# Optimization experiments

Hardware: AMD Instinct MI355X
Metric: run time of the kernel (lower is better)

## Reference

```python
import jax, jax.numpy as jnp
import numpy as np

L, C, B = 256, 20, 1024


def _pos_mask(L):
    # pairwise mask: l2 - l1 >= 1, shape (L, L); broadcast over channels
    ls = jnp.arange(L)
    return (ls[None, :] - ls[:, None]) >= 1


def setup_inputs() -> dict:
    key = jax.random.key(0)
    k0, k1, k2 = jax.random.split(key, 3)
    x_lc = jax.random.uniform(k0, (B, L, C), dtype=jnp.float32)
    theta_0 = jnp.zeros((1,), dtype=jnp.float32)
    theta_lc = jax.random.normal(k1, (1, L, C), dtype=jnp.float32) / np.sqrt(L)
    pm = _pos_mask(L)
    theta_lclc = (jax.random.normal(k2, (1, L, C, L, C), dtype=jnp.float32)
                  / np.sqrt(L * L)) * pm[None, :, None, :, None]
    mask = pm
    return {"x_lc": x_lc, "theta_0": theta_0, "theta_lc": theta_lc,
            "theta_lclc": theta_lclc, "mask": mask}


def reference(x_lc, theta_0, theta_lc, theta_lclc, mask):
    Bn = x_lc.shape[0]
    # additive term: sum_{l,c} theta_lc * x
    phi = theta_0 + jnp.einsum('blc,zlc->b', x_lc, theta_lc)[:, None]
    # pairwise term as a masked bilinear form: x^T (mask * theta) x
    # (avoids materializing the (B,L,C,L,C) broadcast of the original)
    theta_m = theta_lclc[0] * mask[:, None, :, None].astype(theta_lclc.dtype)
    LC = L * C
    xf = x_lc.reshape(Bn, LC)                      # (B, LC)
    tf_ = theta_m.reshape(LC, LC)                  # (LC, LC)
    pair = jnp.einsum('bi,ij,bj->b', xf, tf_, xf)  # two GEMMs under the hood
    phi = phi + pair[:, None]
    return phi
```

## Files before the change

kernel.cpp:

```cpp
#include <hip/hip_runtime.h>
#include <stdint.h>

#define LDIM 256
#define CDIM 20
#define LC   5120
#define NB   1024
#define BM   128
#define BN   256
#define ITOT64 1640

typedef __attribute__((ext_vector_type(8))) short short8;
typedef __attribute__((ext_vector_type(4))) float float4v;
typedef __attribute__((ext_vector_type(4))) unsigned int uint4v;
typedef unsigned short ushort_t;

#define XB_BYTES (10485760ull)
#define WS_NEED  (XB_BYTES)

__device__ inline uint32_t pack_bf16x2(float a, float b) {
    uint32_t ua = __float_as_uint(a);
    uint32_t ub = __float_as_uint(b);
    ua += 0x7fffu + ((ua >> 16) & 1u);
    ub += 0x7fffu + ((ub >> 16) & 1u);
    return (ua >> 16) | (ub & 0xffff0000u);
}

__device__ inline float bf16_to_f32(ushort_t u) {
    return __uint_as_float(((uint32_t)u) << 16);
}

__device__ inline void load_lds16(const void* g, void* l) {
    __builtin_amdgcn_global_load_lds(
        (const __attribute__((address_space(1))) uint32_t*)g,
        (__attribute__((address_space(3))) uint32_t*)l, 16, 0, 0);
}

__global__ __launch_bounds__(256) void xconv_kernel(
    const float* __restrict__ X, const float* __restrict__ th0,
    const float* __restrict__ thlc, ushort_t* __restrict__ Xb,
    float* __restrict__ out)
{
    const int b = blockIdx.x;
    const int t = threadIdx.x;
    __shared__ float red[4];

    const float*  src = X  + (size_t)b * LC;
    ushort_t*     dst = Xb + (size_t)b * LC;
    float s = 0.f;
    for (int c = t * 4; c < LC; c += 1024) {
        float4 f = *(const float4*)(src + c);
        float4 w = *(const float4*)(thlc + c);
        s += f.x * w.x + f.y * w.y + f.z * w.z + f.w * w.w;
        uint2 u;
        u.x = pack_bf16x2(f.x, f.y);
        u.y = pack_bf16x2(f.z, f.w);
        *(uint2*)(dst + c) = u;
    }
    s += __shfl_xor(s, 1);  s += __shfl_xor(s, 2);  s += __shfl_xor(s, 4);
    s += __shfl_xor(s, 8);  s += __shfl_xor(s, 16); s += __shfl_xor(s, 32);
    if ((t & 63) == 0) red[t >> 6] = s;
    __syncthreads();
    if (t == 0) out[b] = th0[0] + red[0] + red[1] + red[2] + red[3];
}

__global__ __launch_bounds__(256, 2) void pair_fused(
    const float* __restrict__ T, const ushort_t* __restrict__ Xb,
    float* __restrict__ out)
{
    const int n    = blockIdx.x;
    const int kblk = ((n >> 3) << 1) | (n & 1);
    const int bn0  = ((n >> 1) & 3) * BN;

    const int gbeg = (ITOT64 * kblk) >> 7;
    const int gend = (ITOT64 * (kblk + 1)) >> 7;

    int it = 0, pre = 0;
    while (pre + (80 - 2 * it) <= gbeg) { pre += 80 - 2 * it; ++it; }
    int li = gbeg - pre;

    __shared__ __align__(16) ushort_t A_s[1024 * 8];
    __shared__ __align__(16) ushort_t B_s[2][2048 * 8];

    const int t    = threadIdx.x;
    const int lane = t & 63;
    const int wid  = t >> 6;
    const int wm   = (wid >> 1) * 64;
    const int wn   = (wid & 1) * 128;
    const int l16  = lane & 15;
    const int qk   = lane >> 4;

    const int r32 = t >> 3;
    const int ga  = t & 7;
    uint32_t offTa[4];
    int      wAdr[4];
    #pragma unroll
    for (int j = 0; j < 4; ++j) {
        const int row = r32 + j * 32;
        offTa[j] = (uint32_t)row * LC + (ga << 3);
        wAdr[j]  = ((row << 3) + (ga ^ (row & 7))) << 4;
    }

    uint32_t offB[8];
    #pragma unroll
    for (int j = 0; j < 8; ++j) {
        const int c = (wid << 9) + (j << 6) + lane;
        const int row = c >> 3;
        const int g2 = (c & 7) ^ (row & 7);
        offB[j] = (uint32_t)(bn0 + row) * LC + (g2 << 3);
    }

    int adrA[2][4], adrB[2][8];
    #pragma unroll
    for (int step = 0; step < 2; ++step) {
        const int kf = step * 4 + qk;
        #pragma unroll
        for (int mt = 0; mt < 4; ++mt) {
            const int r = wm + mt * 16 + l16;
            adrA[step][mt] = ((r << 3) + (kf ^ (r & 7))) << 4;
        }
        #pragma unroll
        for (int nt = 0; nt < 8; ++nt) {
            const int r = wn + nt * 16 + l16;
            adrB[step][nt] = ((r << 3) + (kf ^ (r & 7))) << 4;
        }
    }

    int i0 = it << 7;
    int k0 = i0 + (li << 6);

    float4v acc[4][8];
    #pragma unroll
    for (int mt = 0; mt < 4; ++mt)
        #pragma unroll
        for (int nt = 0; nt < 8; ++nt)
            #pragma unroll
            for (int r = 0; r < 4; ++r) acc[mt][nt][r] = 0.f;

    #pragma unroll
    for (int j = 0; j < 8; ++j)
        load_lds16(Xb + k0 + offB[j], &B_s[0][(((wid << 9) + (j << 6)) << 3)]);

    int cur = 0;

    for (int g = gbeg; g < gend; ++g) {
        const bool haveNext = (g + 1 < gend);
        const int  li_n   = li + 1;
        const bool segEnd = (li_n == 80 - 2 * it);
        const int  it_n   = segEnd ? it + 1 : it;
        const int  i0_n   = it_n << 7;
        const int  k0_n   = segEnd ? i0_n : (k0 + 64);

        const float* Tbase = T + (size_t)i0 * LC + k0;
        float4 a0[4], a1[4];
        #pragma unroll
        for (int j = 0; j < 4; ++j) {
            a0[j] = *(const float4*)(Tbase + offTa[j]);
            a1[j] = *(const float4*)(Tbase + offTa[j] + 4);
        }

        __builtin_amdgcn_sched_barrier(0);
        __builtin_amdgcn_s_barrier();
        __builtin_amdgcn_sched_barrier(0);

        if (haveNext) {
            #pragma unroll
            for (int j = 0; j < 8; ++j)
                load_lds16(Xb + k0_n + offB[j],
                           &B_s[cur ^ 1][(((wid << 9) + (j << 6)) << 3)]);
        }

        #pragma unroll
        for (int j = 0; j < 4; ++j) {
            uint4v v;
            v[0] = pack_bf16x2(a0[j].x, a0[j].y);
            v[1] = pack_bf16x2(a0[j].z, a0[j].w);
            v[2] = pack_bf16x2(a1[j].x, a1[j].y);
            v[3] = pack_bf16x2(a1[j].z, a1[j].w);
            *(uint4v*)((char*)A_s + wAdr[j]) = v;
        }

        asm volatile("s_waitcnt lgkmcnt(0)" ::: "memory");
        __builtin_amdgcn_sched_barrier(0);
        __builtin_amdgcn_s_barrier();
        __builtin_amdgcn_sched_barrier(0);

        const char* Bbase = (const char*)B_s[cur];
        #pragma unroll
        for (int step = 0; step < 2; ++step) {
            short8 af[4], bfr[8];
            #pragma unroll
            for (int mt = 0; mt < 4; ++mt)
                af[mt] = *(const short8*)((const char*)A_s + adrA[step][mt]);
            #pragma unroll
            for (int nt = 0; nt < 8; ++nt)
                bfr[nt] = *(const short8*)(Bbase + adrB[step][nt]);
            __builtin_amdgcn_s_setprio(1);
            #pragma unroll
            for (int mt = 0; mt < 4; ++mt)
                #pragma unroll
                for (int nt = 0; nt < 8; ++nt)
                    acc[mt][nt] = __builtin_amdgcn_mfma_f32_16x16x32_bf16(
                        af[mt], bfr[nt], acc[mt][nt], 0, 0, 0);
            __builtin_amdgcn_s_setprio(0);
        }

        if (segEnd || !haveNext) {
            #pragma unroll
            for (int nt = 0; nt < 8; ++nt) {
                const int b = bn0 + wn + nt * 16 + l16;
                const ushort_t* xb = Xb + (size_t)b * LC + i0 + wm + qk * 4;
                float s = 0.f;
                #pragma unroll
                for (int mt = 0; mt < 4; ++mt) {
                    ushort4 xv = *(const ushort4*)(xb + mt * 16);
                    s += acc[mt][nt][0] * bf16_to_f32(xv.x)
                       + acc[mt][nt][1] * bf16_to_f32(xv.y)
                       + acc[mt][nt][2] * bf16_to_f32(xv.z)
                       + acc[mt][nt][3] * bf16_to_f32(xv.w);
                }
                s += __shfl_xor(s, 16);
                s += __shfl_xor(s, 32);
                if (qk == 0) atomicAdd(&out[b], s);
            }
            #pragma unroll
            for (int mt = 0; mt < 4; ++mt)
                #pragma unroll
                for (int nt = 0; nt < 8; ++nt)
                    #pragma unroll
                    for (int r = 0; r < 4; ++r) acc[mt][nt][r] = 0.f;
        }

        li = segEnd ? 0 : li_n;
        it = it_n;
        i0 = i0_n;
        k0 = k0_n;
        cur ^= 1;
    }
}

__global__ __launch_bounds__(256) void init_kernel(
    const float* __restrict__ x, const float* __restrict__ th0,
    const float* __restrict__ thlc, float* __restrict__ out)
{
    const int b = blockIdx.x;
    const float4* xb = (const float4*)(x + (size_t)b * LC);
    const float4* tv = (const float4*)thlc;
    float s = 0.f;
    for (int i = threadIdx.x; i < LC / 4; i += 256) {
        float4 a = xb[i], t = tv[i];
        s += a.x * t.x + a.y * t.y + a.z * t.z + a.w * t.w;
    }
    s += __shfl_xor(s, 1);  s += __shfl_xor(s, 2);  s += __shfl_xor(s, 4);
    s += __shfl_xor(s, 8);  s += __shfl_xor(s, 16); s += __shfl_xor(s, 32);
    __shared__ float red[4];
    if ((threadIdx.x & 63) == 0) red[threadIdx.x >> 6] = s;
    __syncthreads();
    if (threadIdx.x == 0) out[b] = th0[0] + red[0] + red[1] + red[2] + red[3];
}

__global__ __launch_bounds__(256) void pair_kernel(
    const float* __restrict__ T, const float* __restrict__ X,
    float* __restrict__ out)
{
    const int n  = blockIdx.x;
    const int r  = n & 7;
    const int g  = n >> 3;
    const int i0  = (g >> 3) * BM;
    const int bn0 = (g & 7) * 128;
    const int kstart = i0;
    const int nIter  = (LC - kstart) >> 6;
    const int ipc    = (nIter + 7) >> 3;
    const int itBeg  = r * ipc;
    const int itEnd  = (itBeg + ipc < nIter) ? (itBeg + ipc) : nIter;
    if (itBeg >= itEnd) return;
    const int kbeg   = kstart + (itBeg << 6);

    __shared__ __align__(16) short A_s[8 * BM * 8];
    __shared__ __align__(16) short B_s[8 * BM * 8];

    const int t    = threadIdx.x;
    const int lane = t & 63;
    const int wid  = t >> 6;
    const int wm   = (wid >> 1) * 64;
    const int wn   = (wid & 1) * 64;
    const int l16  = lane & 15;
    const int qk   = lane >> 4;

    const float* pA[4]; const float* pB[4]; int sIdx[4];
    #pragma unroll
    for (int u = 0; u < 4; ++u) {
        const int id  = t + u * 256;
        const int row = id >> 3;
        const int kq  = id & 7;
        pA[u] = T + (size_t)(i0 + row) * LC + kbeg + kq * 8;
        pB[u] = X + (size_t)(bn0 + row) * LC + kbeg + kq * 8;
        sIdx[u] = (kq * BM + (row ^ kq)) * 8;
    }

    float4v acc[4][4] = {};
    for (int itr = itBeg; itr < itEnd; ++itr) {
        __syncthreads();
        #pragma unroll
        for (int u = 0; u < 4; ++u) {
            float4 a0 = ((const float4*)pA[u])[0];
            float4 a1 = ((const float4*)pA[u])[1];
            float4 b0 = ((const float4*)pB[u])[0];
            float4 b1 = ((const float4*)pB[u])[1];
            pA[u] += 64; pB[u] += 64;
            uint4v va, vb;
            va[0] = pack_bf16x2(a0.x, a0.y); va[1] = pack_bf16x2(a0.z, a0.w);
            va[2] = pack_bf16x2(a1.x, a1.y); va[3] = pack_bf16x2(a1.z, a1.w);
            vb[0] = pack_bf16x2(b0.x, b0.y); vb[1] = pack_bf16x2(b0.z, b0.w);
            vb[2] = pack_bf16x2(b1.x, b1.y); vb[3] = pack_bf16x2(b1.z, b1.w);
            *(uint4v*)(A_s + sIdx[u]) = va;
            *(uint4v*)(B_s + sIdx[u]) = vb;
        }
        __syncthreads();
        #pragma unroll
        for (int step = 0; step < 2; ++step) {
            const int kf = step * 4 + qk;
            short8 af[4], bfr[4];
            #pragma unroll
            for (int mt = 0; mt < 4; ++mt)
                af[mt] = *(const short8*)(A_s + (kf * BM + ((wm + mt * 16 + l16) ^ kf)) * 8);
            #pragma unroll
            for (int nt = 0; nt < 4; ++nt)
                bfr[nt] = *(const short8*)(B_s + (kf * BM + ((wn + nt * 16 + l16) ^ kf)) * 8);
            #pragma unroll
            for (int mt = 0; mt < 4; ++mt)
                #pragma unroll
                for (int nt = 0; nt < 4; ++nt)
                    acc[mt][nt] = __builtin_amdgcn_mfma_f32_16x16x32_bf16(
                        af[mt], bfr[nt], acc[mt][nt], 0, 0, 0);
        }
    }
    #pragma unroll
    for (int nt = 0; nt < 4; ++nt) {
        const int b = bn0 + wn + nt * 16 + l16;
        const float* xb = X + (size_t)b * LC + i0 + wm + qk * 4;
        float s = 0.f;
        #pragma unroll
        for (int mt = 0; mt < 4; ++mt) {
            float4 xv = *(const float4*)(xb + mt * 16);
            s += acc[mt][nt][0] * xv.x + acc[mt][nt][1] * xv.y +
                 acc[mt][nt][2] * xv.z + acc[mt][nt][3] * xv.w;
        }
        s += __shfl_xor(s, 16);
        s += __shfl_xor(s, 32);
        if (qk == 0) atomicAdd(&out[b], s);
    }
}

extern "C" void kernel_launch(void* const* d_in, const int* in_sizes, int n_in,
                              void* d_out, int out_size, void* d_ws, size_t ws_size,
                              hipStream_t stream) {
    const float* x    = (const float*)d_in[0];
    const float* th0  = (const float*)d_in[1];
    const float* thlc = (const float*)d_in[2];
    const float* T    = (const float*)d_in[3];
    float* out = (float*)d_out;

    if (ws_size >= WS_NEED) {
        ushort_t* Xb = (ushort_t*)d_ws;
        xconv_kernel<<<NB, 256, 0, stream>>>(x, th0, thlc, Xb, out);
        pair_fused<<<512, 256, 0, stream>>>(T, Xb, out);
    } else {
        init_kernel<<<NB, 256, 0, stream>>>(x, th0, thlc, out);
        pair_kernel<<<(LC / BM) * (NB / 128) * 8, 256, 0, stream>>>(T, x, out);
    }
}
```

Before: 210.4 us.

## Use 512-thread blocks and prefetch next theta tile into registers

The fused pair kernel moves from 512 blocks of 256 threads to 256 blocks of 512 threads. Each of the 8 waves now owns a 64x64 output tile instead of 64x128, which halves per-wave accumulators and per-thread load counts. The fp32 theta tile for the next k-step is loaded into registers one iteration ahead, with a vmcnt wait, so global latency overlaps the MFMA work instead of being exposed each step. Each block's k-range is now twice as long, so there are fewer blocks to spread across CUs and possible load imbalance.

```diff
diff --git a/kernel.cpp b/kernel.cpp
--- a/kernel.cpp
+++ b/kernel.cpp
@@ -63,16 +63,19 @@
     if (t == 0) out[b] = th0[0] + red[0] + red[1] + red[2] + red[3];
 }
 
-__global__ __launch_bounds__(256, 2) void pair_fused(
+__global__ __launch_bounds__(512, 2) void pair_fused(
     const float* __restrict__ T, const ushort_t* __restrict__ Xb,
     float* __restrict__ out)
 {
     const int n    = blockIdx.x;
-    const int kblk = ((n >> 3) << 1) | (n & 1);
-    const int bn0  = ((n >> 1) & 3) * BN;
-
-    const int gbeg = (ITOT64 * kblk) >> 7;
-    const int gend = (ITOT64 * (kblk + 1)) >> 7;
+    const int bcol = (n >> 1) & 3;
+    const int half = n & 1;
+    const int kc   = n >> 3;
+    const int bk64 = kc * 2 + half;
+    const int bn0  = bcol * BN;
+
+    const int gbeg = (ITOT64 * bk64) >> 6;
+    const int gend = (ITOT64 * (bk64 + 1)) >> 6;
 
     int it = 0, pre = 0;
     while (pre + (80 - 2 * it) <= gbeg) { pre += 80 - 2 * it; ++it; }
@@ -84,32 +87,33 @@
     const int t    = threadIdx.x;
     const int lane = t & 63;
     const int wid  = t >> 6;
-    const int wm   = (wid >> 1) * 64;
-    const int wn   = (wid & 1) * 128;
+    const int wm   = (wid >> 2) * 64;
+    const int wn   = (wid & 3) * 64;
     const int l16  = lane & 15;
     const int qk   = lane >> 4;
 
-    const int r32 = t >> 3;
-    const int ga  = t & 7;
-    uint32_t offTa[4];
-    int      wAdr[4];
+    const int ga = t & 7;
+    uint32_t offTa[2];
+    int      wAdr[2];
+    #pragma unroll
+    for (int u = 0; u < 2; ++u) {
+        const int row = (t >> 3) + u * 64;
+        offTa[u] = (uint32_t)row * LC + (ga << 3);
+        wAdr[u]  = ((row << 3) + (ga ^ (row & 7))) << 4;
+    }
+
+    uint32_t offB[4];
+    int      ldsB[4];
     #pragma unroll
     for (int j = 0; j < 4; ++j) {
-        const int row = r32 + j * 32;
-        offTa[j] = (uint32_t)row * LC + (ga << 3);
-        wAdr[j]  = ((row << 3) + (ga ^ (row & 7))) << 4;
-    }
-
-    uint32_t offB[8];
-    #pragma unroll
-    for (int j = 0; j < 8; ++j) {
-        const int c = (wid << 9) + (j << 6) + lane;
+        const int c = (wid << 8) + (j << 6) + lane;
         const int row = c >> 3;
         const int g2 = (c & 7) ^ (row & 7);
         offB[j] = (uint32_t)(bn0 + row) * LC + (g2 << 3);
-    }
-
-    int adrA[2][4], adrB[2][8];
+        ldsB[j] = ((wid << 8) + (j << 6)) << 3;
+    }
+
+    int adrA[2][4], adrB[2][4];
     #pragma unroll
     for (int step = 0; step < 2; ++step) {
         const int kf = step * 4 + qk;
@@ -119,7 +123,7 @@
             adrA[step][mt] = ((r << 3) + (kf ^ (r & 7))) << 4;
         }
         #pragma unroll
-        for (int nt = 0; nt < 8; ++nt) {
+        for (int nt = 0; nt < 4; ++nt) {
             const int r = wn + nt * 16 + l16;
             adrB[step][nt] = ((r << 3) + (kf ^ (r & 7))) << 4;
         }
@@ -128,17 +132,26 @@
     int i0 = it << 7;
     int k0 = i0 + (li << 6);
 
-    float4v acc[4][8];
+    float4v acc[4][4];
     #pragma unroll
     for (int mt = 0; mt < 4; ++mt)
         #pragma unroll
-        for (int nt = 0; nt < 8; ++nt)
+        for (int nt = 0; nt < 4; ++nt)
             #pragma unroll
             for (int r = 0; r < 4; ++r) acc[mt][nt][r] = 0.f;
 
-    #pragma unroll
-    for (int j = 0; j < 8; ++j)
-        load_lds16(Xb + k0 + offB[j], &B_s[0][(((wid << 9) + (j << 6)) << 3)]);
+    float4 a0[2], a1[2];
+    {
+        const float* Tb0 = T + (size_t)i0 * LC + k0;
+        #pragma unroll
+        for (int u = 0; u < 2; ++u) {
+            a0[u] = *(const float4*)(Tb0 + offTa[u]);
+            a1[u] = *(const float4*)(Tb0 + offTa[u] + 4);
+        }
+        #pragma unroll
+        for (int j = 0; j < 4; ++j)
+            load_lds16(Xb + k0 + offB[j], &B_s[0][ldsB[j]]);
+    }
 
     int cur = 0;
 
@@ -150,55 +163,57 @@
         const int  i0_n   = it_n << 7;
         const int  k0_n   = segEnd ? i0_n : (k0 + 64);
 
-        const float* Tbase = T + (size_t)i0 * LC + k0;
-        float4 a0[4], a1[4];
-        #pragma unroll
-        for (int j = 0; j < 4; ++j) {
-            a0[j] = *(const float4*)(Tbase + offTa[j]);
-            a1[j] = *(const float4*)(Tbase + offTa[j] + 4);
-        }
-
         __builtin_amdgcn_sched_barrier(0);
         __builtin_amdgcn_s_barrier();
         __builtin_amdgcn_sched_barrier(0);
 
+        #pragma unroll
+        for (int u = 0; u < 2; ++u) {
+            uint4v v;
+            v[0] = pack_bf16x2(a0[u].x, a0[u].y);
+            v[1] = pack_bf16x2(a0[u].z, a0[u].w);
+            v[2] = pack_bf16x2(a1[u].x, a1[u].y);
+            v[3] = pack_bf16x2(a1[u].z, a1[u].w);
+            *(uint4v*)((char*)A_s + wAdr[u]) = v;
+        }
+
         if (haveNext) {
-            #pragma unroll
-            for (int j = 0; j < 8; ++j)
-                load_lds16(Xb + k0_n + offB[j],
-                           &B_s[cur ^ 1][(((wid << 9) + (j << 6)) << 3)]);
-        }
-
-        #pragma unroll
-        for (int j = 0; j < 4; ++j) {
-            uint4v v;
-            v[0] = pack_bf16x2(a0[j].x, a0[j].y);
-            v[1] = pack_bf16x2(a0[j].z, a0[j].w);
-            v[2] = pack_bf16x2(a1[j].x, a1[j].y);
-            v[3] = pack_bf16x2(a1[j].z, a1[j].w);
-            *(uint4v*)((char*)A_s + wAdr[j]) = v;
+            const float* Tb2 = T + (size_t)i0_n * LC + k0_n;
+            #pragma unroll
+            for (int u = 0; u < 2; ++u) {
+                a0[u] = *(const float4*)(Tb2 + offTa[u]);
+                a1[u] = *(const float4*)(Tb2 + offTa[u] + 4);
+            }
+            #pragma unroll
+            for (int j = 0; j < 4; ++j)
+                load_lds16(Xb + k0_n + offB[j], &B_s[cur ^ 1][ldsB[j]]);
         }
 
         asm volatile("s_waitcnt lgkmcnt(0)" ::: "memory");
         __builtin_amdgcn_sched_barrier(0);
+        if (haveNext)
+            asm volatile("s_waitcnt vmcnt(8)" ::: "memory");
+        else
+            asm volatile("s_waitcnt vmcnt(0)" ::: "memory");
+        __builtin_amdgcn_sched_barrier(0);
         __builtin_amdgcn_s_barrier();
         __builtin_amdgcn_sched_barrier(0);
 
         const char* Bbase = (const char*)B_s[cur];
         #pragma unroll
         for (int step = 0; step < 2; ++step) {
-            short8 af[4], bfr[8];
+            short8 af[4], bfr[4];
             #pragma unroll
             for (int mt = 0; mt < 4; ++mt)
                 af[mt] = *(const short8*)((const char*)A_s + adrA[step][mt]);
             #pragma unroll
-            for (int nt = 0; nt < 8; ++nt)
+            for (int nt = 0; nt < 4; ++nt)
                 bfr[nt] = *(const short8*)(Bbase + adrB[step][nt]);
             __builtin_amdgcn_s_setprio(1);
             #pragma unroll
             for (int mt = 0; mt < 4; ++mt)
                 #pragma unroll
-                for (int nt = 0; nt < 8; ++nt)
+                for (int nt = 0; nt < 4; ++nt)
                     acc[mt][nt] = __builtin_amdgcn_mfma_f32_16x16x32_bf16(
                         af[mt], bfr[nt], acc[mt][nt], 0, 0, 0);
             __builtin_amdgcn_s_setprio(0);
@@ -206,7 +221,7 @@
 
         if (segEnd || !haveNext) {
             #pragma unroll
-            for (int nt = 0; nt < 8; ++nt) {
+            for (int nt = 0; nt < 4; ++nt) {
                 const int b = bn0 + wn + nt * 16 + l16;
                 const ushort_t* xb = Xb + (size_t)b * LC + i0 + wm + qk * 4;
                 float s = 0.f;
@@ -225,7 +240,7 @@
             #pragma unroll
             for (int mt = 0; mt < 4; ++mt)
                 #pragma unroll
-                for (int nt = 0; nt < 8; ++nt)
+                for (int nt = 0; nt < 4; ++nt)
                     #pragma unroll
                     for (int r = 0; r < 4; ++r) acc[mt][nt][r] = 0.f;
         }
@@ -363,7 +378,7 @@
     if (ws_size >= WS_NEED) {
         ushort_t* Xb = (ushort_t*)d_ws;
         xconv_kernel<<<NB, 256, 0, stream>>>(x, th0, thlc, Xb, out);
-        pair_fused<<<512, 256, 0, stream>>>(T, Xb, out);
+        pair_fused<<<256, 512, 0, stream>>>(T, Xb, out);
     } else {
         init_kernel<<<NB, 256, 0, stream>>>(x, th0, thlc, out);
         pair_kernel<<<(LC / BM) * (NB / 128) * 8, 256, 0, stream>>>(T, x, out);
```

Result: slower. 220.7 us (+4.9%).
